# Optimization experiments

Measured on AMD Instinct MI355X. Metric: run time of the kernel, lower is better.

The kernel has to match this reference:

```python
import jax, jax.numpy as jnp
import numpy as np

N = 100000      # nodes
E = 1600000     # edges (before self-loops)
F_IN = 512      # input features
H = 8           # heads layer 1
D = 8           # per-head dim layer 1
C = 40          # classes (layer 2 out, heads=1)
NEG_SLOPE = 0.2 # PyG GATConv default negative_slope


def setup_inputs() -> dict:
    key = jax.random.key(0)
    ks = jax.random.split(key, 10)
    x = jax.random.normal(ks[0], (N, F_IN), jnp.float32)
    edge_index = jax.random.randint(ks[1], (2, E), 0, N, dtype=jnp.int32)
    W1 = jax.random.normal(ks[2], (F_IN, H * D), jnp.float32) / np.float32(np.sqrt(F_IN))
    att_src1 = jax.random.normal(ks[3], (H, D), jnp.float32) / np.float32(np.sqrt(D))
    att_dst1 = jax.random.normal(ks[4], (H, D), jnp.float32) / np.float32(np.sqrt(D))
    b1 = jnp.zeros((H * D,), jnp.float32)
    W2 = jax.random.normal(ks[5], (H * D, C), jnp.float32) / np.float32(np.sqrt(H * D))
    att_src2 = jax.random.normal(ks[6], (1, C), jnp.float32) / np.float32(np.sqrt(C))
    att_dst2 = jax.random.normal(ks[7], (1, C), jnp.float32) / np.float32(np.sqrt(C))
    b2 = jnp.zeros((C,), jnp.float32)
    return {"x": x, "edge_index": edge_index, "W1": W1, "att_src1": att_src1,
            "att_dst1": att_dst1, "b1": b1, "W2": W2, "att_src2": att_src2,
            "att_dst2": att_dst2, "b2": b2}


def _gat_layer(x, src, dst, W, a_src, a_dst, heads, dim):
    # Dense projection, then per-head attention logits.
    h = (x @ W).reshape(-1, heads, dim)            # [N, H, D]
    alpha_s = jnp.einsum('nhd,hd->nh', h, a_src)   # [N, H]
    alpha_d = jnp.einsum('nhd,hd->nh', h, a_dst)
    e = jax.nn.leaky_relu(alpha_s[src] + alpha_d[dst], NEG_SLOPE)  # [E, H]
    # Segment softmax over edges grouped by destination node.
    emax = jax.ops.segment_max(e, dst, num_segments=N)
    emax = jnp.where(jnp.isfinite(emax), emax, 0.0)
    ee = jnp.exp(e - emax[dst])
    denom = jax.ops.segment_sum(ee, dst, num_segments=N)
    alpha = ee / (denom[dst] + 1e-16)              # [E, H]
    # Scatter-aggregate weighted neighbor features.
    msg = h[src] * alpha[:, :, None]               # [E, H, D]
    return jax.ops.segment_sum(msg, dst, num_segments=N)  # [N, H, D]


def reference(x, edge_index, W1, att_src1, att_dst1, b1, W2, att_src2, att_dst2, b2):
    # PyG GATConv adds self-loops by default.
    loops = jnp.arange(N, dtype=edge_index.dtype)
    src = jnp.concatenate([edge_index[0], loops])
    dst = jnp.concatenate([edge_index[1], loops])
    # Layer 1: 8 heads, concat=True, then ELU. (dropouts identity in eval mode)
    h1 = _gat_layer(x, src, dst, W1, att_src1, att_dst1, H, D).reshape(N, H * D) + b1
    h1 = jax.nn.elu(h1)
    # Layer 2: 1 head, concat=False -> mean over heads (trivial for H=1).
    h2 = _gat_layer(h1, src, dst, W2, att_src2, att_dst2, 1, C)[:, 0, :] + b2
    return jax.nn.log_softmax(h2, axis=1)
```

## Files before the change

### kernel.cpp

```cpp
#include <hip/hip_runtime.h>

#define F_IN   512
#define HD     64
#define NHEAD  8
#define NC     40
#define NEG    0.2f

typedef __attribute__((ext_vector_type(8))) short bf16x8;
typedef __attribute__((ext_vector_type(4))) float f32x4;

__device__ __forceinline__ float lrelu(float x) { return x > 0.0f ? x : NEG * x; }

__device__ __forceinline__ short f2bf(float f) {
    unsigned u = __float_as_uint(f);
    u += 0x7FFF + ((u >> 16) & 1);
    return (short)(u >> 16);
}
__device__ __forceinline__ float bf2f(short h) {
    return __uint_as_float(((unsigned)(unsigned short)h) << 16);
}
__device__ __forceinline__ float bfl(unsigned u) { return __uint_as_float(u << 16); }
__device__ __forceinline__ float bfh(unsigned u) { return __uint_as_float(u & 0xFFFF0000u); }

__global__ void zero_kernel(int* __restrict__ p, int n) {
    int i = blockIdx.x * 256 + threadIdx.x;
    if (i < n) p[i] = 0;
}

__global__ __launch_bounds__(256) void scanA_kernel(const int* __restrict__ deg,
                                                    int* __restrict__ incl,
                                                    int* __restrict__ bsum, int Nn) {
    __shared__ int wsum[4];
    int t = threadIdx.x, b = blockIdx.x;
    int base = b * 1024 + t * 4;
    int v0 = (base + 0) < Nn ? deg[base + 0] : 0;
    int v1 = (base + 1) < Nn ? deg[base + 1] : 0;
    int v2 = (base + 2) < Nn ? deg[base + 2] : 0;
    int v3 = (base + 3) < Nn ? deg[base + 3] : 0;
    int p0 = v0, p1 = p0 + v1, p2 = p1 + v2, p3 = p2 + v3;
    int lane = t & 63, w = t >> 6;
    int sc = p3;
    for (int off = 1; off < 64; off <<= 1) {
        int u = __shfl_up(sc, off);
        if (lane >= off) sc += u;
    }
    if (lane == 63) wsum[w] = sc;
    __syncthreads();
    int woff = 0;
#pragma unroll
    for (int i = 0; i < 4; ++i) if (i < w) woff += wsum[i];
    int excl = woff + sc - p3;
    if (base + 0 < Nn) incl[base + 0] = excl + p0;
    if (base + 1 < Nn) incl[base + 1] = excl + p1;
    if (base + 2 < Nn) incl[base + 2] = excl + p2;
    if (base + 3 < Nn) incl[base + 3] = excl + p3;
    if (t == 0) bsum[b] = wsum[0] + wsum[1] + wsum[2] + wsum[3];
}

__global__ void scanB_kernel(int* __restrict__ bsum, int nb) {
    int lane = threadIdx.x;
    int a = lane < nb ? bsum[lane] : 0;
    int c = (lane + 64) < nb ? bsum[lane + 64] : 0;
    int sa = a, sc2 = c;
    for (int off = 1; off < 64; off <<= 1) {
        int u = __shfl_up(sa, off);  if (lane >= off) sa += u;
        int u2 = __shfl_up(sc2, off); if (lane >= off) sc2 += u2;
    }
    int totA = __shfl(sa, 63);
    int ea = sa - a;
    int ec = totA + sc2 - c;
    if (lane < nb) bsum[lane] = ea;
    if (lane + 64 < nb) bsum[lane + 64] = ec;
}

__global__ void scanC_kernel(const int* __restrict__ incl, const int* __restrict__ bsum,
                             int* __restrict__ rp, int Nn) {
    int i = blockIdx.x * 256 + threadIdx.x;
    if (i == 0) rp[0] = 0;
    if (i < Nn) rp[i + 1] = incl[i] + bsum[i >> 10];
}

__global__ void scatter_kernel(const int* __restrict__ src, const int* __restrict__ dst,
                               const int* __restrict__ pos, const int* __restrict__ rp,
                               int* __restrict__ col, int E) {
    int e = blockIdx.x * 256 + threadIdx.x;
    if (e < E) {
        int d = dst[e];
        col[rp[d] + pos[e]] = src[e];
    }
}

__global__ void wsplit_kernel(const float* __restrict__ W, short* __restrict__ Whp,
                              short* __restrict__ Wlp) {
    int t = blockIdx.x * 256 + threadIdx.x;
    if (t >= F_IN * HD) return;
    int k = t >> 6, c = t & 63;
    float wv = W[t];
    short hh = f2bf(wv);
    int idx = (((k >> 3) * 64 + c) << 3) + (k & 7);
    Whp[idx] = hh;
    Wlp[idx] = f2bf(wv - bf2f(hh));
}

#define G1_BM 64
__global__ __launch_bounds__(256) void g1c_kernel(const float* __restrict__ X,
                                                  const short* __restrict__ Whp,
                                                  const short* __restrict__ Wlp,
                                                  const float* __restrict__ att_s,
                                                  const float* __restrict__ att_d,
                                                  unsigned short* __restrict__ Hp,
                                                  float* __restrict__ as1,
                                                  float* __restrict__ ad1,
                                                  const int* __restrict__ dst,
                                                  int* __restrict__ deg,
                                                  int* __restrict__ pos,
                                                  int Nn, int E, int nG1) {
    int tid = threadIdx.x;

    if ((int)blockIdx.x >= nG1) {
        int e = ((int)blockIdx.x - nG1) * 256 + tid;
        if (e < E) pos[e] = atomicAdd(&deg[dst[e]], 1);
        return;
    }

    int wid = tid >> 6, lane = tid & 63;
    int lrow = lane & 15, kgrp = lane >> 4;
    int row0 = blockIdx.x * G1_BM;
    int rowA = row0 + wid * 16 + lrow;

    float ats[4], atd[4];
#pragma unroll
    for (int fc = 0; fc < 4; ++fc) { ats[fc] = att_s[fc * 16 + lrow]; atd[fc] = att_d[fc * 16 + lrow]; }

    f32x4 acc[4];
#pragma unroll
    for (int fc = 0; fc < 4; ++fc) acc[fc] = (f32x4){0.f, 0.f, 0.f, 0.f};

    bool valid = rowA < Nn;
    const float* xrow = X + (size_t)rowA * F_IN + kgrp * 8;
    const bf16x8* WhV = reinterpret_cast<const bf16x8*>(Whp);
    const bf16x8* WlV = reinterpret_cast<const bf16x8*>(Wlp);

    float4 a_cur[2], a_nxt[2];
    if (valid) {
        a_cur[0] = *reinterpret_cast<const float4*>(xrow);
        a_cur[1] = *reinterpret_cast<const float4*>(xrow + 4);
    } else {
        a_cur[0] = a_cur[1] = make_float4(0.f, 0.f, 0.f, 0.f);
    }

#pragma unroll 2
    for (int it = 0; it < F_IN / 32; ++it) {
        if (it + 1 < F_IN / 32) {
            if (valid) {
                const float* p = xrow + (it + 1) * 32;
                a_nxt[0] = *reinterpret_cast<const float4*>(p);
                a_nxt[1] = *reinterpret_cast<const float4*>(p + 4);
            } else {
                a_nxt[0] = a_nxt[1] = make_float4(0.f, 0.f, 0.f, 0.f);
            }
        }
        bf16x8 af;
        {
            float fs[8] = {a_cur[0].x, a_cur[0].y, a_cur[0].z, a_cur[0].w,
                           a_cur[1].x, a_cur[1].y, a_cur[1].z, a_cur[1].w};
#pragma unroll
            for (int j = 0; j < 8; ++j) af[j] = f2bf(fs[j]);
        }
        const bf16x8* bhp = WhV + (size_t)(it * 4 + kgrp) * 64;
        const bf16x8* blp = WlV + (size_t)(it * 4 + kgrp) * 64;
#pragma unroll
        for (int fc = 0; fc < 4; ++fc) {
            bf16x8 bh = bhp[fc * 16 + lrow];
            bf16x8 bl = blp[fc * 16 + lrow];
            acc[fc] = __builtin_amdgcn_mfma_f32_16x16x32_bf16(af, bh, acc[fc], 0, 0, 0);
            acc[fc] = __builtin_amdgcn_mfma_f32_16x16x32_bf16(af, bl, acc[fc], 0, 0, 0);
        }
        a_cur[0] = a_nxt[0];
        a_cur[1] = a_nxt[1];
    }

#pragma unroll
    for (int r = 0; r < 4; ++r) {
        int gr = row0 + wid * 16 + kgrp * 4 + r;
        float hv[4], sp[4], dp[4];
#pragma unroll
        for (int fc = 0; fc < 4; ++fc) {
            hv[fc] = acc[fc][r];
            sp[fc] = hv[fc] * ats[fc];
            dp[fc] = hv[fc] * atd[fc];
        }
#pragma unroll
        for (int mask = 1; mask <= 4; mask <<= 1) {
#pragma unroll
            for (int fc = 0; fc < 4; ++fc) {
                sp[fc] += __shfl_xor(sp[fc], mask);
                dp[fc] += __shfl_xor(dp[fc], mask);
            }
        }
        if (gr < Nn) {
#pragma unroll
            for (int fc = 0; fc < 4; ++fc)
                Hp[(size_t)gr * HD + fc * 16 + lrow] = (unsigned short)f2bf(hv[fc]);
            if ((lane & 7) == 0) {
                int hh = lrow >> 3;
#pragma unroll
                for (int fc = 0; fc < 4; ++fc) {
                    as1[gr * NHEAD + fc * 2 + hh] = sp[fc];
                    ad1[gr * NHEAD + fc * 2 + hh] = dp[fc];
                }
            }
        }
    }
}

__global__ __launch_bounds__(256) void agg1_kernel(const unsigned short* __restrict__ Hp,
                                                   const float* __restrict__ as1,
                                                   const float* __restrict__ ad1,
                                                   const int* __restrict__ col,
                                                   const int* __restrict__ rp,
                                                   const float* __restrict__ b1,
                                                   float* __restrict__ h1, int Nn) {
    int n = blockIdx.x * 4 + (threadIdx.x >> 6);
    int lane = threadIdx.x & 63;
    if (n >= Nn) return;
    int slot = lane >> 3, j = lane & 7;
    int beg = rp[n], end = rp[n + 1];
    float adv1 = ad1[n * NHEAD + j];
    float acc[8] = {0, 0, 0, 0, 0, 0, 0, 0};
    float dw = 0.f;
    for (int t = beg + slot; t < end; t += 8) {
        int s = col[t];
        float w = __expf(lrelu(as1[s * NHEAD + j] + adv1));
        dw += w;
        uint4 u = *reinterpret_cast<const uint4*>(&Hp[(size_t)s * HD + j * 8]);
        acc[0] += w * bfl(u.x); acc[1] += w * bfh(u.x);
        acc[2] += w * bfl(u.y); acc[3] += w * bfh(u.y);
        acc[4] += w * bfl(u.z); acc[5] += w * bfh(u.z);
        acc[6] += w * bfl(u.w); acc[7] += w * bfh(u.w);
    }
#pragma unroll
    for (int mask = 8; mask < 64; mask <<= 1) {
#pragma unroll
        for (int i = 0; i < 8; ++i) acc[i] += __shfl_xor(acc[i], mask);
        dw += __shfl_xor(dw, mask);
    }
    float w = __expf(lrelu(as1[n * NHEAD + j] + adv1));
    uint4 u = *reinterpret_cast<const uint4*>(&Hp[(size_t)n * HD + j * 8]);
    acc[0] += w * bfl(u.x); acc[1] += w * bfh(u.x);
    acc[2] += w * bfl(u.y); acc[3] += w * bfh(u.y);
    acc[4] += w * bfl(u.z); acc[5] += w * bfh(u.z);
    acc[6] += w * bfl(u.w); acc[7] += w * bfh(u.w);
    dw += w;
    float invd = 1.0f / (dw + 1e-16f);
    float4 b0 = *reinterpret_cast<const float4*>(&b1[j * 8]);
    float4 b4 = *reinterpret_cast<const float4*>(&b1[j * 8 + 4]);
    float bb[8] = {b0.x, b0.y, b0.z, b0.w, b4.x, b4.y, b4.z, b4.w};
#pragma unroll
    for (int i = 0; i < 8; ++i) {
        float v = acc[i] * invd + bb[i];
        acc[i] = v > 0.0f ? v : __expf(v) - 1.0f;
    }
    if (slot == 0) {
        float4 o0 = make_float4(acc[0], acc[1], acc[2], acc[3]);
        float4 o1 = make_float4(acc[4], acc[5], acc[6], acc[7]);
        *reinterpret_cast<float4*>(&h1[(size_t)n * HD + j * 8]) = o0;
        *reinterpret_cast<float4*>(&h1[(size_t)n * HD + j * 8 + 4]) = o1;
    }
}

#define G2R 64
__global__ __launch_bounds__(256) void gemm2_kernel(const float* __restrict__ H1,
                                                    const float* __restrict__ W2,
                                                    const float* __restrict__ asw,
                                                    const float* __restrict__ adw,
                                                    unsigned int* __restrict__ h2p,
                                                    float* __restrict__ as2,
                                                    float* __restrict__ ad2, int Nn) {
    __shared__ float Hs[G2R][HD + 1];
    __shared__ float W2s[HD][NC];
    __shared__ float asv[NC], adv[NC];
    int tid = threadIdx.x;
    for (int i = tid; i < HD * NC; i += 256) W2s[i / NC][i % NC] = W2[i];
    if (tid < NC) { asv[tid] = asw[tid]; adv[tid] = adw[tid]; }
    int row0 = blockIdx.x * G2R;
#pragma unroll
    for (int i = 0; i < 4; ++i) {
        int linear = i * 1024 + tid * 4;
        int r = linear >> 6, c = linear & 63;
        int gr = row0 + r;
        float4 v = make_float4(0.f, 0.f, 0.f, 0.f);
        if (gr < Nn) v = *reinterpret_cast<const float4*>(&H1[(size_t)gr * HD + c]);
        Hs[r][c + 0] = v.x; Hs[r][c + 1] = v.y; Hs[r][c + 2] = v.z; Hs[r][c + 3] = v.w;
    }
    __syncthreads();
    int row = tid >> 2, cg = tid & 3;
    int gr = row0 + row;
    float acc[10];
#pragma unroll
    for (int jj = 0; jj < 10; ++jj) acc[jj] = 0.0f;
    for (int k = 0; k < HD; ++k) {
        float a = Hs[row][k];
#pragma unroll
        for (int jj = 0; jj < 10; ++jj) acc[jj] += a * W2s[k][cg * 10 + jj];
    }
    float sa = 0.0f, da = 0.0f;
#pragma unroll
    for (int jj = 0; jj < 10; ++jj) {
        sa += acc[jj] * asv[cg * 10 + jj];
        da += acc[jj] * adv[cg * 10 + jj];
    }
    sa += __shfl_xor(sa, 1); sa += __shfl_xor(sa, 2);
    da += __shfl_xor(da, 1); da += __shfl_xor(da, 2);
    if (gr < Nn) {
        if (cg == 0) { as2[gr] = sa; ad2[gr] = da; }
#pragma unroll
        for (int jj = 0; jj < 5; ++jj) {
            unsigned int u = ((unsigned int)(unsigned short)f2bf(acc[2 * jj + 1]) << 16) |
                             (unsigned short)f2bf(acc[2 * jj]);
            h2p[(size_t)gr * 20 + cg * 5 + jj] = u;
        }
    }
}

__global__ __launch_bounds__(256) void agg2_kernel(const unsigned int* __restrict__ h2p,
                                                   const float* __restrict__ as2,
                                                   const float* __restrict__ ad2,
                                                   const int* __restrict__ col,
                                                   const int* __restrict__ rp,
                                                   const float* __restrict__ b2,
                                                   float* __restrict__ out, int Nn) {
    int n = blockIdx.x * 4 + (threadIdx.x >> 6);
    int lane = threadIdx.x & 63;
    if (n >= Nn) return;
    int slot = lane >> 4, l16 = lane & 15;
    bool act = l16 < 10;
    int beg = rp[n], end = rp[n + 1];
    float adv = ad2[n];
    float4 acc = make_float4(0.f, 0.f, 0.f, 0.f);
    float dw = 0.f;
    for (int t = beg + slot; t < end; t += 4) {
        int s = col[t];
        float w = __expf(lrelu(as2[s] + adv));
        dw += w;
        if (act) {
            uint2 u = *reinterpret_cast<const uint2*>(&h2p[(size_t)s * 20 + l16 * 2]);
            acc.x += w * bfl(u.x); acc.y += w * bfh(u.x);
            acc.z += w * bfl(u.y); acc.w += w * bfh(u.y);
        }
    }
#pragma unroll
    for (int mask = 16; mask < 64; mask <<= 1) {
        acc.x += __shfl_xor(acc.x, mask);
        acc.y += __shfl_xor(acc.y, mask);
        acc.z += __shfl_xor(acc.z, mask);
        acc.w += __shfl_xor(acc.w, mask);
        dw    += __shfl_xor(dw, mask);
    }
    float w = __expf(lrelu(as2[n] + adv));
    dw += w;
    float invd = 1.0f / (dw + 1e-16f);
    if (act) {
        uint2 u = *reinterpret_cast<const uint2*>(&h2p[(size_t)n * 20 + l16 * 2]);
        float4 bb = *reinterpret_cast<const float4*>(&b2[l16 * 4]);
        acc.x = (acc.x + w * bfl(u.x)) * invd + bb.x;
        acc.y = (acc.y + w * bfh(u.x)) * invd + bb.y;
        acc.z = (acc.z + w * bfl(u.y)) * invd + bb.z;
        acc.w = (acc.w + w * bfh(u.y)) * invd + bb.w;
    }
    float mloc = act ? fmaxf(fmaxf(acc.x, acc.y), fmaxf(acc.z, acc.w)) : -INFINITY;
#pragma unroll
    for (int mask = 1; mask < 16; mask <<= 1) mloc = fmaxf(mloc, __shfl_xor(mloc, mask));
    float s4 = act ? (__expf(acc.x - mloc) + __expf(acc.y - mloc) +
                      __expf(acc.z - mloc) + __expf(acc.w - mloc)) : 0.0f;
#pragma unroll
    for (int mask = 1; mask < 16; mask <<= 1) s4 += __shfl_xor(s4, mask);
    float lse = mloc + __logf(s4);
    if (slot == 0 && act) {
        float4 o = make_float4(acc.x - lse, acc.y - lse, acc.z - lse, acc.w - lse);
        *reinterpret_cast<float4*>(&out[(size_t)n * NC + l16 * 4]) = o;
    }
}

extern "C" void kernel_launch(void* const* d_in, const int* in_sizes, int n_in,
                              void* d_out, int out_size, void* d_ws, size_t ws_size,
                              hipStream_t stream) {
    const float* x    = (const float*)d_in[0];
    const int*   ei   = (const int*)d_in[1];
    const float* W1   = (const float*)d_in[2];
    const float* as1w = (const float*)d_in[3];
    const float* ad1w = (const float*)d_in[4];
    const float* b1   = (const float*)d_in[5];
    const float* W2   = (const float*)d_in[6];
    const float* as2w = (const float*)d_in[7];
    const float* ad2w = (const float*)d_in[8];
    const float* b2   = (const float*)d_in[9];
    float* out = (float*)d_out;

    int Nn = in_sizes[0] / F_IN;
    int E  = in_sizes[1] / 2;
    const int* srcv = ei;
    const int* dstv = ei + E;

    char* ws = (char*)d_ws;
    size_t off = 0;
    auto alloc = [&](size_t bytes) { size_t cur = off; off += (bytes + 255) & ~255ULL; return cur; };
    unsigned short* Hp = (unsigned short*)(ws + alloc((size_t)Nn * HD * 2));
    float* h1   = (float*)(ws + alloc((size_t)Nn * HD * 4));
    float* as1v = (float*)(ws + alloc((size_t)Nn * NHEAD * 4));
    float* ad1v = (float*)(ws + alloc((size_t)Nn * NHEAD * 4));
    unsigned int* h2p = (unsigned int*)(ws + alloc((size_t)Nn * 20 * 4));
    float* as2v = (float*)(ws + alloc((size_t)Nn * 4));
    float* ad2v = (float*)(ws + alloc((size_t)Nn * 4));
    int* deg  = (int*)(ws + alloc((size_t)Nn * 4));
    int* incl = (int*)(ws + alloc((size_t)Nn * 4));
    int* rp   = (int*)(ws + alloc((size_t)(Nn + 1) * 4));
    int* pos  = (int*)(ws + alloc((size_t)E * 4));
    int* col  = (int*)(ws + alloc((size_t)E * 4));
    int* bsum = (int*)(ws + alloc(256 * 4));
    short* Whp = (short*)(ws + alloc((size_t)F_IN * HD * 2));
    short* Wlp = (short*)(ws + alloc((size_t)F_IN * HD * 2));

    int nb   = (Nn + 1023) / 1024;
    int nG1  = (Nn + G1_BM - 1) / G1_BM;
    int nCNT = (E + 255) / 256;

    zero_kernel<<<(Nn + 255) / 256, 256, 0, stream>>>(deg, Nn);
    wsplit_kernel<<<(F_IN * HD + 255) / 256, 256, 0, stream>>>(W1, Whp, Wlp);
    g1c_kernel<<<nG1 + nCNT, 256, 0, stream>>>(x, Whp, Wlp, as1w, ad1w, Hp, as1v, ad1v,
                                               dstv, deg, pos, Nn, E, nG1);
    scanA_kernel<<<nb, 256, 0, stream>>>(deg, incl, bsum, Nn);
    scanB_kernel<<<1, 64, 0, stream>>>(bsum, nb);
    scanC_kernel<<<(Nn + 255) / 256, 256, 0, stream>>>(incl, bsum, rp, Nn);
    scatter_kernel<<<(E + 255) / 256, 256, 0, stream>>>(srcv, dstv, pos, rp, col, E);

    agg1_kernel<<<(Nn + 3) / 4, 256, 0, stream>>>(Hp, as1v, ad1v, col, rp, b1, h1, Nn);
    gemm2_kernel<<<(Nn + G2R - 1) / G2R, 256, 0, stream>>>(h1, W2, as2w, ad2w, h2p, as2v, ad2v, Nn);
    agg2_kernel<<<(Nn + 3) / 4, 256, 0, stream>>>(h2p, as2v, ad2v, col, rp, b2, out, Nn);
}
```

Measured before the change: 351.4 us.

## Drop low-part weight split in layer-1 GEMM, double rows per wave, prefetch deeper

The layer-1 projection stops using the hi/lo bf16 split of W1, which halves the MFMA count and weight loads. Each wave now computes 32 rows instead of 16 (block tile 128), so each weight fragment is reused across two row fragments. X loads are prefetched two iterations ahead and weight fragments one iteration ahead. This lowers the precision of the projection to plain bf16 weights, which may hurt accuracy, and raises register use.

```diff
diff --git a/kernel.cpp b/kernel.cpp
--- a/kernel.cpp
+++ b/kernel.cpp
@@ -90,22 +90,16 @@
     }
 }
 
-__global__ void wsplit_kernel(const float* __restrict__ W, short* __restrict__ Whp,
-                              short* __restrict__ Wlp) {
+__global__ void wconv_kernel(const float* __restrict__ W, short* __restrict__ Whp) {
     int t = blockIdx.x * 256 + threadIdx.x;
     if (t >= F_IN * HD) return;
     int k = t >> 6, c = t & 63;
-    float wv = W[t];
-    short hh = f2bf(wv);
-    int idx = (((k >> 3) * 64 + c) << 3) + (k & 7);
-    Whp[idx] = hh;
-    Wlp[idx] = f2bf(wv - bf2f(hh));
-}
-
-#define G1_BM 64
+    Whp[((((k >> 3) * 64 + c)) << 3) + (k & 7)] = f2bf(W[t]);
+}
+
+#define G1_BM 128
 __global__ __launch_bounds__(256) void g1c_kernel(const float* __restrict__ X,
                                                   const short* __restrict__ Whp,
-                                                  const short* __restrict__ Wlp,
                                                   const float* __restrict__ att_s,
                                                   const float* __restrict__ att_d,
                                                   unsigned short* __restrict__ Hp,
@@ -126,88 +120,107 @@
     int wid = tid >> 6, lane = tid & 63;
     int lrow = lane & 15, kgrp = lane >> 4;
     int row0 = blockIdx.x * G1_BM;
-    int rowA = row0 + wid * 16 + lrow;
+    int rowA = row0 + wid * 32 + lrow;
 
     float ats[4], atd[4];
 #pragma unroll
     for (int fc = 0; fc < 4; ++fc) { ats[fc] = att_s[fc * 16 + lrow]; atd[fc] = att_d[fc * 16 + lrow]; }
 
-    f32x4 acc[4];
-#pragma unroll
-    for (int fc = 0; fc < 4; ++fc) acc[fc] = (f32x4){0.f, 0.f, 0.f, 0.f};
-
-    bool valid = rowA < Nn;
-    const float* xrow = X + (size_t)rowA * F_IN + kgrp * 8;
+    f32x4 acc[2][4];
+#pragma unroll
+    for (int fr = 0; fr < 2; ++fr)
+#pragma unroll
+        for (int fc = 0; fc < 4; ++fc) acc[fr][fc] = (f32x4){0.f, 0.f, 0.f, 0.f};
+
+    bool v0 = rowA < Nn, v1 = (rowA + 16) < Nn;
+    const float* x0 = X + (size_t)rowA * F_IN + kgrp * 8;
+    const float* x1 = x0 + (size_t)16 * F_IN;
     const bf16x8* WhV = reinterpret_cast<const bf16x8*>(Whp);
-    const bf16x8* WlV = reinterpret_cast<const bf16x8*>(Wlp);
-
-    float4 a_cur[2], a_nxt[2];
-    if (valid) {
-        a_cur[0] = *reinterpret_cast<const float4*>(xrow);
-        a_cur[1] = *reinterpret_cast<const float4*>(xrow + 4);
-    } else {
-        a_cur[0] = a_cur[1] = make_float4(0.f, 0.f, 0.f, 0.f);
-    }
-
-#pragma unroll 2
+
+    const float4 z4 = make_float4(0.f, 0.f, 0.f, 0.f);
+    float4 ac[2][2], a1[2][2], a2[2][2];
+    bf16x8 bc[4], bn[4];
+
+    ac[0][0] = v0 ? *reinterpret_cast<const float4*>(x0)     : z4;
+    ac[0][1] = v0 ? *reinterpret_cast<const float4*>(x0 + 4) : z4;
+    ac[1][0] = v1 ? *reinterpret_cast<const float4*>(x1)     : z4;
+    ac[1][1] = v1 ? *reinterpret_cast<const float4*>(x1 + 4) : z4;
+    a1[0][0] = v0 ? *reinterpret_cast<const float4*>(x0 + 32)     : z4;
+    a1[0][1] = v0 ? *reinterpret_cast<const float4*>(x0 + 36) : z4;
+    a1[1][0] = v1 ? *reinterpret_cast<const float4*>(x1 + 32)     : z4;
+    a1[1][1] = v1 ? *reinterpret_cast<const float4*>(x1 + 36) : z4;
+    {
+        const bf16x8* bp = WhV + (size_t)kgrp * 64;
+#pragma unroll
+        for (int fc = 0; fc < 4; ++fc) bc[fc] = bp[fc * 16 + lrow];
+    }
+
+#pragma unroll
     for (int it = 0; it < F_IN / 32; ++it) {
+        if (it + 2 < F_IN / 32) {
+            const float* p0 = x0 + (it + 2) * 32;
+            const float* p1 = x1 + (it + 2) * 32;
+            a2[0][0] = v0 ? *reinterpret_cast<const float4*>(p0)     : z4;
+            a2[0][1] = v0 ? *reinterpret_cast<const float4*>(p0 + 4) : z4;
+            a2[1][0] = v1 ? *reinterpret_cast<const float4*>(p1)     : z4;
+            a2[1][1] = v1 ? *reinterpret_cast<const float4*>(p1 + 4) : z4;
+        }
         if (it + 1 < F_IN / 32) {
-            if (valid) {
-                const float* p = xrow + (it + 1) * 32;
-                a_nxt[0] = *reinterpret_cast<const float4*>(p);
-                a_nxt[1] = *reinterpret_cast<const float4*>(p + 4);
-            } else {
-                a_nxt[0] = a_nxt[1] = make_float4(0.f, 0.f, 0.f, 0.f);
+            const bf16x8* bp = WhV + (size_t)((it + 1) * 4 + kgrp) * 64;
+#pragma unroll
+            for (int fc = 0; fc < 4; ++fc) bn[fc] = bp[fc * 16 + lrow];
+        }
+#pragma unroll
+        for (int fr = 0; fr < 2; ++fr) {
+            float fs[8] = {ac[fr][0].x, ac[fr][0].y, ac[fr][0].z, ac[fr][0].w,
+                           ac[fr][1].x, ac[fr][1].y, ac[fr][1].z, ac[fr][1].w};
+            bf16x8 af;
+#pragma unroll
+            for (int j = 0; j < 8; ++j) af[j] = f2bf(fs[j]);
+#pragma unroll
+            for (int fc = 0; fc < 4; ++fc)
+                acc[fr][fc] = __builtin_amdgcn_mfma_f32_16x16x32_bf16(af, bc[fc], acc[fr][fc], 0, 0, 0);
+        }
+#pragma unroll
+        for (int fr = 0; fr < 2; ++fr) {
+            ac[fr][0] = a1[fr][0]; ac[fr][1] = a1[fr][1];
+            a1[fr][0] = a2[fr][0]; a1[fr][1] = a2[fr][1];
+        }
+#pragma unroll
+        for (int fc = 0; fc < 4; ++fc) bc[fc] = bn[fc];
+    }
+
+#pragma unroll
+    for (int fr = 0; fr < 2; ++fr) {
+#pragma unroll
+        for (int r = 0; r < 4; ++r) {
+            int gr = row0 + wid * 32 + fr * 16 + kgrp * 4 + r;
+            float hv[4], sp[4], dp[4];
+#pragma unroll
+            for (int fc = 0; fc < 4; ++fc) {
+                hv[fc] = acc[fr][fc][r];
+                sp[fc] = hv[fc] * ats[fc];
+                dp[fc] = hv[fc] * atd[fc];
             }
-        }
-        bf16x8 af;
-        {
-            float fs[8] = {a_cur[0].x, a_cur[0].y, a_cur[0].z, a_cur[0].w,
-                           a_cur[1].x, a_cur[1].y, a_cur[1].z, a_cur[1].w};
-#pragma unroll
-            for (int j = 0; j < 8; ++j) af[j] = f2bf(fs[j]);
-        }
-        const bf16x8* bhp = WhV + (size_t)(it * 4 + kgrp) * 64;
-        const bf16x8* blp = WlV + (size_t)(it * 4 + kgrp) * 64;
-#pragma unroll
-        for (int fc = 0; fc < 4; ++fc) {
-            bf16x8 bh = bhp[fc * 16 + lrow];
-            bf16x8 bl = blp[fc * 16 + lrow];
-            acc[fc] = __builtin_amdgcn_mfma_f32_16x16x32_bf16(af, bh, acc[fc], 0, 0, 0);
-            acc[fc] = __builtin_amdgcn_mfma_f32_16x16x32_bf16(af, bl, acc[fc], 0, 0, 0);
-        }
-        a_cur[0] = a_nxt[0];
-        a_cur[1] = a_nxt[1];
-    }
-
-#pragma unroll
-    for (int r = 0; r < 4; ++r) {
-        int gr = row0 + wid * 16 + kgrp * 4 + r;
-        float hv[4], sp[4], dp[4];
-#pragma unroll
-        for (int fc = 0; fc < 4; ++fc) {
-            hv[fc] = acc[fc][r];
-            sp[fc] = hv[fc] * ats[fc];
-            dp[fc] = hv[fc] * atd[fc];
-        }
-#pragma unroll
-        for (int mask = 1; mask <= 4; mask <<= 1) {
-#pragma unroll
-            for (int fc = 0; fc < 4; ++fc) {
-                sp[fc] += __shfl_xor(sp[fc], mask);
-                dp[fc] += __shfl_xor(dp[fc], mask);
+#pragma unroll
+            for (int mask = 1; mask <= 4; mask <<= 1) {
+#pragma unroll
+                for (int fc = 0; fc < 4; ++fc) {
+                    sp[fc] += __shfl_xor(sp[fc], mask);
+                    dp[fc] += __shfl_xor(dp[fc], mask);
+                }
             }
-        }
-        if (gr < Nn) {
-#pragma unroll
-            for (int fc = 0; fc < 4; ++fc)
-                Hp[(size_t)gr * HD + fc * 16 + lrow] = (unsigned short)f2bf(hv[fc]);
-            if ((lane & 7) == 0) {
-                int hh = lrow >> 3;
-#pragma unroll
-                for (int fc = 0; fc < 4; ++fc) {
-                    as1[gr * NHEAD + fc * 2 + hh] = sp[fc];
-                    ad1[gr * NHEAD + fc * 2 + hh] = dp[fc];
+            if (gr < Nn) {
+#pragma unroll
+                for (int fc = 0; fc < 4; ++fc)
+                    Hp[(size_t)gr * HD + fc * 16 + lrow] = (unsigned short)f2bf(hv[fc]);
+                if ((lane & 7) == 0) {
+                    int hh = lrow >> 3;
+#pragma unroll
+                    for (int fc = 0; fc < 4; ++fc) {
+                        as1[gr * NHEAD + fc * 2 + hh] = sp[fc];
+                        ad1[gr * NHEAD + fc * 2 + hh] = dp[fc];
+                    }
                 }
             }
         }
@@ -419,15 +432,14 @@
     int* col  = (int*)(ws + alloc((size_t)E * 4));
     int* bsum = (int*)(ws + alloc(256 * 4));
     short* Whp = (short*)(ws + alloc((size_t)F_IN * HD * 2));
-    short* Wlp = (short*)(ws + alloc((size_t)F_IN * HD * 2));
 
     int nb   = (Nn + 1023) / 1024;
     int nG1  = (Nn + G1_BM - 1) / G1_BM;
     int nCNT = (E + 255) / 256;
 
     zero_kernel<<<(Nn + 255) / 256, 256, 0, stream>>>(deg, Nn);
-    wsplit_kernel<<<(F_IN * HD + 255) / 256, 256, 0, stream>>>(W1, Whp, Wlp);
-    g1c_kernel<<<nG1 + nCNT, 256, 0, stream>>>(x, Whp, Wlp, as1w, ad1w, Hp, as1v, ad1v,
+    wconv_kernel<<<(F_IN * HD + 255) / 256, 256, 0, stream>>>(W1, Whp);
+    g1c_kernel<<<nG1 + nCNT, 256, 0, stream>>>(x, Whp, as1w, ad1w, Hp, as1v, ad1v,
                                                dstv, deg, pos, Nn, E, nG1);
     scanA_kernel<<<nb, 256, 0, stream>>>(deg, incl, bsum, Nn);
     scanB_kernel<<<1, 64, 0, stream>>>(bsum, nb);
```

New measurement: 375.1 us. +6.7%, slower.
